# Performance work log

Measured on AMD Instinct MI355X. Metric: run time of the kernel, lower is better.

## Reference

```python
import jax, jax.numpy as jnp
import numpy as np

NP_, NS_ = 100000, 10000      # num pdrugs / seffect nodes
FPD, FSE = 512, 768           # raw feature dims
H = 64                        # hidden_channels
E = 1_600_000                 # message-passing edges
L = 1_000_000                 # labeled edges (pos+neg)


def setup_inputs() -> dict:
    key = jax.random.key(0)
    ks = jax.random.split(key, 40)
    f32 = jnp.float32

    def nrm(k, shape, scale=0.05):
        return jax.random.normal(k, shape, f32) * scale

    inp = {}
    inp['x_pdrugs'] = jax.random.normal(ks[0], (NP_, FPD), f32)
    inp['x_seffect'] = jax.random.normal(ks[1], (NS_, FSE), f32)
    inp['node_id_pd'] = jnp.arange(NP_)
    inp['node_id_se'] = jnp.arange(NS_)
    inp['edge_index'] = jnp.stack([
        jax.random.randint(ks[2], (E,), 0, NP_),
        jax.random.randint(ks[3], (E,), 0, NS_)])
    # positive labeled edges + negative-sampled edges (label 0)
    inp['edge_label_index'] = jnp.stack([
        jax.random.randint(ks[4], (L,), 0, NP_),
        jax.random.randint(ks[5], (L,), 0, NS_)])
    inp['edge_label'] = jnp.concatenate(
        [jnp.ones(L // 2, f32), jnp.zeros(L - L // 2, f32)])

    # input projections + node embeddings
    inp['W_pd'] = nrm(ks[6], (FPD, H)); inp['b_pd'] = jnp.zeros((H,), f32)
    inp['W_se'] = nrm(ks[7], (FSE, H)); inp['b_se'] = jnp.zeros((H,), f32)
    inp['emb_pd'] = nrm(ks[8], (NP_, H), 1.0)
    inp['emb_se'] = nrm(ks[9], (NS_, H), 1.0)

    # hetero SAGEConv params: 2 layers x 2 edge types (p2s, s2p)
    i = 10
    for lyr in (1, 2):
        for et in ('p2s', 's2p'):
            inp[f'c{lyr}_{et}_Wl'] = nrm(ks[i], (H, H)); i += 1
            inp[f'c{lyr}_{et}_bl'] = jnp.zeros((H,), f32)
            inp[f'c{lyr}_{et}_Wr'] = nrm(ks[i], (H, H)); i += 1
    return inp


def _sage(x_src, x_dst, src_idx, dst_idx, n_dst, Wl, bl, Wr):
    # SAGEConv: lin_l(mean_j x_src[j]) + lin_r(x_dst)
    msg = x_src[src_idx]                                   # [E, H] gather
    agg = jax.ops.segment_sum(msg, dst_idx, num_segments=n_dst)
    deg = jax.ops.segment_sum(jnp.ones((src_idx.shape[0],), x_src.dtype),
                              dst_idx, num_segments=n_dst)
    mean = agg / jnp.clip(deg, 1.0)[:, None]
    return mean @ Wl + bl + x_dst @ Wr


def reference(x_pdrugs, x_seffect, edge_label,
              W_pd, b_pd, W_se, b_se, emb_pd, emb_se,
              c1_p2s_Wl, c1_p2s_bl, c1_p2s_Wr,
              c1_s2p_Wl, c1_s2p_bl, c1_s2p_Wr,
              c2_p2s_Wl, c2_p2s_bl, c2_p2s_Wr,
              c2_s2p_Wl, c2_s2p_bl, c2_s2p_Wr,
              node_id_pd, node_id_se, edge_index, edge_label_index):
    src, dst = edge_index[0], edge_index[1]  # pdrugs -> seffect

    # embed + linear fusion
    h_pd = x_pdrugs @ W_pd + b_pd + emb_pd[node_id_pd]
    h_se = x_seffect @ W_se + b_se + emb_se[node_id_se]

    # hetero GNN layer 1 (relu)
    se1 = jax.nn.relu(_sage(h_pd, h_se, src, dst, NS_, c1_p2s_Wl, c1_p2s_bl, c1_p2s_Wr))
    pd1 = jax.nn.relu(_sage(h_se, h_pd, dst, src, NP_, c1_s2p_Wl, c1_s2p_bl, c1_s2p_Wr))

    # hetero GNN layer 2 (no activation)
    se2 = _sage(pd1, se1, src, dst, NS_, c2_p2s_Wl, c2_p2s_bl, c2_p2s_Wr)
    pd2 = _sage(se1, pd1, dst, src, NP_, c2_s2p_Wl, c2_s2p_bl, c2_s2p_Wr)

    # edge-wise gather-dot classifier
    pred = jnp.sum(pd2[edge_label_index[0]] * se2[edge_label_index[1]], axis=-1)
    return (pred, edge_label)
```

## Files before the change

kernel.cpp:

```cpp
#include <hip/hip_runtime.h>

namespace {

constexpr int NP = 100000;
constexpr int NS = 10000;
constexpr int EC = 1600000;
constexpr int LC = 1000000;

constexpr int SH_S = 6;
constexpr int SH_P = 9;
constexpr int NBS = (NS + 63) >> SH_S;
constexpr int NBP = (NP + 511) >> SH_P;
constexpr int CHUNK = 8192;
constexpr int NBLK = (EC + CHUNK - 1) / CHUNK;

typedef short i16x8 __attribute__((ext_vector_type(8)));
typedef float f32x4 __attribute__((ext_vector_type(4)));

__device__ inline ushort f2bf(float f) {
  unsigned u = __float_as_uint(f);
  u += 0x7FFFu + ((u >> 16) & 1u);
  return (ushort)(u >> 16);
}


__global__ void __launch_bounds__(256) k_bcount(const int* __restrict__ src,
                                                const int* __restrict__ dst,
                                                int* __restrict__ bcntS,
                                                int* __restrict__ bcntP, int E) {
  __shared__ int hS[256];
  __shared__ int hP[256];
  const int t = threadIdx.x;
  hS[t] = 0;
  hP[t] = 0;
  __syncthreads();
  const int base = blockIdx.x * CHUNK;
  const int end = min(base + CHUNK, E);
  for (int e = base + t; e < end; e += 256) {
    atomicAdd(&hS[dst[e] >> SH_S], 1);
    atomicAdd(&hP[src[e] >> SH_P], 1);
  }
  __syncthreads();
  if (t < NBS && hS[t]) atomicAdd(&bcntS[t], hS[t]);
  if (t < NBP && hP[t]) atomicAdd(&bcntP[t], hP[t]);
}

__global__ void __launch_bounds__(256) k_bscan(const int* __restrict__ bcntS,
                                               const int* __restrict__ bcntP,
                                               int* __restrict__ gbaseS,
                                               int* __restrict__ gbaseP,
                                               int* __restrict__ gcurS,
                                               int* __restrict__ gcurP) {
  __shared__ int s[256];
  const int t = threadIdx.x;
  int v = (t < NBS) ? bcntS[t] : 0;
  s[t] = v;
  __syncthreads();
  for (int off = 1; off < 256; off <<= 1) {
    int u = (t >= off) ? s[t - off] : 0;
    __syncthreads();
    s[t] += u;
    __syncthreads();
  }
  if (t < NBS) {
    int ex = s[t] - v;
    gbaseS[t] = ex;
    gcurS[t] = ex;
  }
  __syncthreads();
  v = (t < NBP) ? bcntP[t] : 0;
  s[t] = v;
  __syncthreads();
  for (int off = 1; off < 256; off <<= 1) {
    int u = (t >= off) ? s[t - off] : 0;
    __syncthreads();
    s[t] += u;
    __syncthreads();
  }
  if (t < NBP) {
    int ex = s[t] - v;
    gbaseP[t] = ex;
    gcurP[t] = ex;
  }
}

__global__ void __launch_bounds__(256) k_bscatter(const int* __restrict__ src,
                                                  const int* __restrict__ dst,
                                                  int* __restrict__ gcurS,
                                                  int* __restrict__ gcurP,
                                                  int2* __restrict__ tmpS,
                                                  int2* __restrict__ tmpP, int E) {
  __shared__ int hS[256];
  __shared__ int hP[256];
  const int t = threadIdx.x;
  hS[t] = 0;
  hP[t] = 0;
  __syncthreads();
  const int base = blockIdx.x * CHUNK;
  const int end = min(base + CHUNK, E);
  for (int e = base + t; e < end; e += 256) {
    atomicAdd(&hS[dst[e] >> SH_S], 1);
    atomicAdd(&hP[src[e] >> SH_P], 1);
  }
  __syncthreads();
  int myBaseS = 0, myBaseP = 0;
  if (t < NBS) {
    int c = hS[t];
    myBaseS = c ? atomicAdd(&gcurS[t], c) : 0;
  }
  if (t < NBP) {
    int c = hP[t];
    myBaseP = c ? atomicAdd(&gcurP[t], c) : 0;
  }
  __syncthreads();
  if (t < NBS) hS[t] = myBaseS;
  if (t < NBP) hP[t] = myBaseP;
  __syncthreads();
  for (int e = base + t; e < end; e += 256) {
    const int d = dst[e];
    const int s = src[e];
    int p = atomicAdd(&hS[d >> SH_S], 1);
    tmpS[p] = make_int2(d, s);
    int q = atomicAdd(&hP[s >> SH_P], 1);
    tmpP[q] = make_int2(s, d);
  }
}

template <int NN>
__global__ void __launch_bounds__(256) k_bfinal(const int2* __restrict__ tmp,
                                                const int* __restrict__ gbase,
                                                const int* __restrict__ bcnt,
                                                int shift, int Nnodes,
                                                int* __restrict__ rowptr,
                                                int* __restrict__ deg,
                                                int* __restrict__ col) {
  __shared__ int ldeg[NN];
  __shared__ int lscan[512];
  const int b = blockIdx.x;
  const int t = threadIdx.x;
  const int n0 = b << shift;
  const int base = gbase[b];
  const int cnt = bcnt[b];
  for (int i = t; i < NN; i += 256) ldeg[i] = 0;
  __syncthreads();
  for (int j = t; j < cnt; j += 256) atomicAdd(&ldeg[tmp[base + j].x - n0], 1);
  __syncthreads();
  for (int i = t; i < 512; i += 256) lscan[i] = (i < NN) ? ldeg[i] : 0;
  __syncthreads();
  for (int off = 1; off < 512; off <<= 1) {
    const int i0 = t, i1 = t + 256;
    const int v0 = (i0 >= off) ? lscan[i0 - off] : 0;
    const int v1 = (i1 >= off) ? lscan[i1 - off] : 0;
    __syncthreads();
    lscan[i0] += v0;
    lscan[i1] += v1;
    __syncthreads();
  }
  for (int i = t; i < NN; i += 256) {
    const int n = n0 + i;
    if (n < Nnodes) {
      const int dg = ldeg[i];
      rowptr[n] = base + lscan[i] - dg;
      deg[n] = dg;
    }
  }
  __syncthreads();
  for (int i = t; i < NN; i += 256) lscan[i] -= ldeg[i];
  __syncthreads();
  for (int j = t; j < cnt; j += 256) {
    const int2 pr = tmp[base + j];
    const int p = atomicAdd(&lscan[pr.x - n0], 1);
    col[base + p] = pr.y;
  }
}


struct WtJob {
  const float* src;
  ushort* dst;
  int K;
  int stride;
  int off;
};
struct WtJobs {
  WtJob j[10];
};

__global__ void __launch_bounds__(256) k_wt_all(WtJobs jobs) {
  int e = blockIdx.x * 256 + threadIdx.x;
#pragma unroll
  for (int i = 0; i < 10; i++) {
    const int K = jobs.j[i].K;
    const int sz = K * 64;
    if (e < sz) {
      const int n = e / K;
      const int k = e - n * K;
      jobs.j[i].dst[(size_t)n * jobs.j[i].stride + jobs.j[i].off + k] =
          f2bf(jobs.j[i].src[(size_t)k * 64 + n]);
      return;
    }
    e -= sz;
  }
}


template <bool RELU, bool EMB>
__global__ void __launch_bounds__(256) k_mgemm(const float* __restrict__ A0,
                                               const float* __restrict__ A1, int KA0,
                                               int sA0, int sA1, int K,
                                               const ushort* __restrict__ Wt,
                                               const float* __restrict__ bias,
                                               const float* __restrict__ emb,
                                               const int* __restrict__ nid,
                                               float* __restrict__ out, int M) {
  __shared__ ushort Xs[64 * 72];
  __shared__ ushort Ws[64 * 72];
  const int t = threadIdx.x;
  const int row0 = blockIdx.x * 64;
  const int lane = t & 63;
  const int w = t >> 6;
  const int m16 = lane & 15;
  const int q = lane >> 4;

  f32x4 acc[4];
#pragma unroll
  for (int nt = 0; nt < 4; nt++) acc[nt] = {0.f, 0.f, 0.f, 0.f};

  const int ksteps = K >> 6;
  for (int ks = 0; ks < ksteps; ks++) {
    const int k0 = ks << 6;
    float4 xv[4];
#pragma unroll
    for (int i = 0; i < 4; i++) {
      const int u = t + i * 256;
      const int row = u >> 4;
      const int k4 = (u & 15) << 2;
      const int gr = min(row0 + row, M - 1);
      const int kk = k0 + k4;
      const float* sp = (kk < KA0) ? (A0 + (size_t)gr * sA0 + kk)
                                   : (A1 + (size_t)gr * sA1 + (kk - KA0));
      xv[i] = *reinterpret_cast<const float4*>(sp);
    }
    uint4 wv[2];
#pragma unroll
    for (int i = 0; i < 2; i++) {
      const int u = t + i * 256;
      const int n = u >> 3;
      const int kk8 = (u & 7) << 3;
      wv[i] = *reinterpret_cast<const uint4*>(Wt + (size_t)n * K + k0 + kk8);
    }
    __syncthreads();
#pragma unroll
    for (int i = 0; i < 4; i++) {
      const int u = t + i * 256;
      const int row = u >> 4;
      const int k4 = (u & 15) << 2;
      ushort4 o;
      o.x = f2bf(xv[i].x);
      o.y = f2bf(xv[i].y);
      o.z = f2bf(xv[i].z);
      o.w = f2bf(xv[i].w);
      *reinterpret_cast<ushort4*>(&Xs[row * 72 + k4]) = o;
    }
#pragma unroll
    for (int i = 0; i < 2; i++) {
      const int u = t + i * 256;
      const int n = u >> 3;
      const int kk8 = (u & 7) << 3;
      *reinterpret_cast<uint4*>(&Ws[n * 72 + kk8]) = wv[i];
    }
    __syncthreads();

    const ushort* ap = &Xs[(w * 16 + m16) * 72 + q * 8];
    const i16x8 a0 = *reinterpret_cast<const i16x8*>(ap);
    const i16x8 a1 = *reinterpret_cast<const i16x8*>(ap + 32);
#pragma unroll
    for (int nt = 0; nt < 4; nt++) {
      const ushort* bp = &Ws[(nt * 16 + m16) * 72 + q * 8];
      const i16x8 b0 = *reinterpret_cast<const i16x8*>(bp);
      const i16x8 b1 = *reinterpret_cast<const i16x8*>(bp + 32);
      acc[nt] = __builtin_amdgcn_mfma_f32_16x16x32_bf16(a0, b0, acc[nt], 0, 0, 0);
      acc[nt] = __builtin_amdgcn_mfma_f32_16x16x32_bf16(a1, b1, acc[nt], 0, 0, 0);
    }
  }

  int grow[4];
  int nrow[4];
#pragma unroll
  for (int r = 0; r < 4; r++) {
    grow[r] = row0 + w * 16 + q * 4 + r;
    nrow[r] = (EMB && grow[r] < M) ? nid[grow[r]] : 0;
  }
#pragma unroll
  for (int nt = 0; nt < 4; nt++) {
    const int colv = nt * 16 + m16;
    const float bv = bias[colv];
#pragma unroll
    for (int r = 0; r < 4; r++) {
      if (grow[r] < M) {
        float v = acc[nt][r] + bv;
        if (EMB) v += emb[(size_t)nrow[r] * 64 + colv];
        if (RELU) v = fmaxf(v, 0.f);
        out[(size_t)grow[r] * 64 + colv] = v;
      }
    }
  }
}


__global__ void __launch_bounds__(256) k_agg(const float* __restrict__ h,
                                             const int* __restrict__ rowptr,
                                             const int* __restrict__ deg,
                                             const int* __restrict__ col,
                                             float* __restrict__ mean, int n_dst) {
  const int node = blockIdx.x * 4 + (threadIdx.x >> 6);
  const int lane = threadIdx.x & 63;
  if (node >= n_dst) return;
  const int beg = rowptr[node];
  const int cnt = deg[node];
  float acc = 0.f;
  int j = 0;
  for (; j + 8 <= cnt; j += 8) {
    int n0 = col[beg + j + 0], n1 = col[beg + j + 1];
    int n2 = col[beg + j + 2], n3 = col[beg + j + 3];
    int n4 = col[beg + j + 4], n5 = col[beg + j + 5];
    int n6 = col[beg + j + 6], n7 = col[beg + j + 7];
    float a0 = h[(size_t)n0 * 64 + lane];
    float a1 = h[(size_t)n1 * 64 + lane];
    float a2 = h[(size_t)n2 * 64 + lane];
    float a3 = h[(size_t)n3 * 64 + lane];
    float a4 = h[(size_t)n4 * 64 + lane];
    float a5 = h[(size_t)n5 * 64 + lane];
    float a6 = h[(size_t)n6 * 64 + lane];
    float a7 = h[(size_t)n7 * 64 + lane];
    acc += ((a0 + a1) + (a2 + a3)) + ((a4 + a5) + (a6 + a7));
  }
  for (; j < cnt; ++j) acc += h[(size_t)col[beg + j] * 64 + lane];
  const float d = (cnt > 0) ? (float)cnt : 1.f;
  mean[(size_t)node * 64 + lane] = acc / d;
}


__global__ void __launch_bounds__(256) k_classify(const float* __restrict__ pd2,
                                                  const float* __restrict__ se2,
                                                  const int* __restrict__ i0,
                                                  const int* __restrict__ i1,
                                                  float* __restrict__ pred, int L) {
  const int e = blockIdx.x * 16 + (threadIdx.x >> 4);
  if (e >= L) return;
  const int l16 = threadIdx.x & 15;
  const int a = i0[e];
  const int b = i1[e];
  const float4 va = *reinterpret_cast<const float4*>(&pd2[(size_t)a * 64 + l16 * 4]);
  const float4 vb = *reinterpret_cast<const float4*>(&se2[(size_t)b * 64 + l16 * 4]);
  float v = va.x * vb.x + va.y * vb.y + va.z * vb.z + va.w * vb.w;
  v += __shfl_xor(v, 1, 16);
  v += __shfl_xor(v, 2, 16);
  v += __shfl_xor(v, 4, 16);
  v += __shfl_xor(v, 8, 16);
  if (l16 == 0) pred[e] = v;
}

__global__ void k_copy4(const float4* __restrict__ src, float4* __restrict__ dst, int n4) {
  int i = blockIdx.x * blockDim.x + threadIdx.x;
  if (i < n4) dst[i] = src[i];
}

}

extern "C" void kernel_launch(void* const* d_in, const int* in_sizes, int n_in,
                              void* d_out, int out_size, void* d_ws, size_t ws_size,
                              hipStream_t stream) {
  (void)in_sizes; (void)n_in; (void)out_size; (void)ws_size;
  const float* x_pd = (const float*)d_in[0];
  const float* x_se = (const float*)d_in[1];
  const int* nid_pd = (const int*)d_in[2];
  const int* nid_se = (const int*)d_in[3];
  const int* eidx = (const int*)d_in[4];
  const int* elidx = (const int*)d_in[5];
  const float* elabel = (const float*)d_in[6];
  const float* W_pd = (const float*)d_in[7];
  const float* b_pd = (const float*)d_in[8];
  const float* W_se = (const float*)d_in[9];
  const float* b_se = (const float*)d_in[10];
  const float* emb_pd = (const float*)d_in[11];
  const float* emb_se = (const float*)d_in[12];
  const float* c1_p2s_Wl = (const float*)d_in[13];
  const float* c1_p2s_bl = (const float*)d_in[14];
  const float* c1_p2s_Wr = (const float*)d_in[15];
  const float* c1_s2p_Wl = (const float*)d_in[16];
  const float* c1_s2p_bl = (const float*)d_in[17];
  const float* c1_s2p_Wr = (const float*)d_in[18];
  const float* c2_p2s_Wl = (const float*)d_in[19];
  const float* c2_p2s_bl = (const float*)d_in[20];
  const float* c2_p2s_Wr = (const float*)d_in[21];
  const float* c2_s2p_Wl = (const float*)d_in[22];
  const float* c2_s2p_bl = (const float*)d_in[23];
  const float* c2_s2p_Wr = (const float*)d_in[24];

  const int* src = eidx;
  const int* dst = eidx + EC;
  const int* li0 = elidx;
  const int* li1 = elidx + LC;

  char* ws = (char*)d_ws;
  size_t o = 0;
  auto alloc = [&](size_t bytes) -> char* {
    char* p = ws + o;
    o = (o + bytes + 255) & ~(size_t)255;
    return p;
  };
  float* h_pd = (float*)alloc((size_t)NP * 64 * 4);
  float* h_se = (float*)alloc((size_t)NS * 64 * 4);
  float* pd1 = (float*)alloc((size_t)NP * 64 * 4);
  float* se1 = (float*)alloc((size_t)NS * 64 * 4);
  float* agg_pd = (float*)alloc((size_t)NP * 64 * 4);
  float* agg_se = (float*)alloc((size_t)NS * 64 * 4);
  int* col_se = (int*)alloc((size_t)EC * 4);
  int* col_pd = (int*)alloc((size_t)EC * 4);
  int* deg_se = (int*)alloc((size_t)NS * 4);
  int* deg_pd = (int*)alloc((size_t)NP * 4);
  int* rp_se = (int*)alloc((size_t)NS * 4);
  int* rp_pd = (int*)alloc((size_t)NP * 4);
  int* bcntS = (int*)alloc(1024);
  int* bcntP = (int*)alloc(1024);
  int* gbaseS = (int*)alloc(1024);
  int* gbaseP = (int*)alloc(1024);
  int* gcurS = (int*)alloc(1024);
  int* gcurP = (int*)alloc(1024);
  ushort* wt_pd = (ushort*)alloc((size_t)64 * 512 * 2);
  ushort* wt_se = (ushort*)alloc((size_t)64 * 768 * 2);
  ushort* wt_c1p2s = (ushort*)alloc((size_t)64 * 128 * 2);
  ushort* wt_c1s2p = (ushort*)alloc((size_t)64 * 128 * 2);
  ushort* wt_c2p2s = (ushort*)alloc((size_t)64 * 128 * 2);
  ushort* wt_c2s2p = (ushort*)alloc((size_t)64 * 128 * 2);

  int2* tmpS = (int2*)agg_pd;
  int2* tmpP = tmpS + EC;

  hipMemsetAsync(bcntS, 0, 1024, stream);
  hipMemsetAsync(bcntP, 0, 1024, stream);

  k_bcount<<<NBLK, 256, 0, stream>>>(src, dst, bcntS, bcntP, EC);
  k_bscan<<<1, 256, 0, stream>>>(bcntS, bcntP, gbaseS, gbaseP, gcurS, gcurP);
  k_bscatter<<<NBLK, 256, 0, stream>>>(src, dst, gcurS, gcurP, tmpS, tmpP, EC);
  k_bfinal<64><<<NBS, 256, 0, stream>>>(tmpS, gbaseS, bcntS, SH_S, NS, rp_se, deg_se, col_se);
  k_bfinal<512><<<NBP, 256, 0, stream>>>(tmpP, gbaseP, bcntP, SH_P, NP, rp_pd, deg_pd, col_pd);

  {
    WtJobs jobs;
    jobs.j[0] = {W_pd, wt_pd, 512, 512, 0};
    jobs.j[1] = {W_se, wt_se, 768, 768, 0};
    jobs.j[2] = {c1_p2s_Wl, wt_c1p2s, 64, 128, 0};
    jobs.j[3] = {c1_p2s_Wr, wt_c1p2s, 64, 128, 64};
    jobs.j[4] = {c1_s2p_Wl, wt_c1s2p, 64, 128, 0};
    jobs.j[5] = {c1_s2p_Wr, wt_c1s2p, 64, 128, 64};
    jobs.j[6] = {c2_p2s_Wl, wt_c2p2s, 64, 128, 0};
    jobs.j[7] = {c2_p2s_Wr, wt_c2p2s, 64, 128, 64};
    jobs.j[8] = {c2_s2p_Wl, wt_c2s2p, 64, 128, 0};
    jobs.j[9] = {c2_s2p_Wr, wt_c2s2p, 64, 128, 64};
    const int tot = 64 * (512 + 768 + 8 * 64);
    k_wt_all<<<(tot + 255) / 256, 256, 0, stream>>>(jobs);
  }

  const int gP = (NP + 63) / 64;
  const int gS = (NS + 63) / 64;

  k_mgemm<false, true><<<gP, 256, 0, stream>>>(x_pd, nullptr, 512, 512, 0, 512, wt_pd,
                                               b_pd, emb_pd, nid_pd, h_pd, NP);
  k_mgemm<false, true><<<gS, 256, 0, stream>>>(x_se, nullptr, 768, 768, 0, 768, wt_se,
                                               b_se, emb_se, nid_se, h_se, NS);

  k_agg<<<(NS + 3) / 4, 256, 0, stream>>>(h_pd, rp_se, deg_se, col_se, agg_se, NS);
  k_mgemm<true, false><<<gS, 256, 0, stream>>>(agg_se, h_se, 64, 64, 64, 128, wt_c1p2s,
                                               c1_p2s_bl, nullptr, nullptr, se1, NS);
  k_agg<<<(NP + 3) / 4, 256, 0, stream>>>(h_se, rp_pd, deg_pd, col_pd, agg_pd, NP);
  k_mgemm<true, false><<<gP, 256, 0, stream>>>(agg_pd, h_pd, 64, 64, 64, 128, wt_c1s2p,
                                               c1_s2p_bl, nullptr, nullptr, pd1, NP);

  float* se2 = h_se;
  float* pd2 = h_pd;
  k_agg<<<(NS + 3) / 4, 256, 0, stream>>>(pd1, rp_se, deg_se, col_se, agg_se, NS);
  k_mgemm<false, false><<<gS, 256, 0, stream>>>(agg_se, se1, 64, 64, 64, 128, wt_c2p2s,
                                                c2_p2s_bl, nullptr, nullptr, se2, NS);
  k_agg<<<(NP + 3) / 4, 256, 0, stream>>>(se1, rp_pd, deg_pd, col_pd, agg_pd, NP);
  k_mgemm<false, false><<<gP, 256, 0, stream>>>(agg_pd, pd1, 64, 64, 64, 128, wt_c2s2p,
                                                c2_s2p_bl, nullptr, nullptr, pd2, NP);

  float* outF = (float*)d_out;
  k_classify<<<(LC + 15) / 16, 256, 0, stream>>>(pd2, se2, li0, li1, outF, LC);
  k_copy4<<<(LC / 4 + 255) / 256, 256, 0, stream>>>((const float4*)elabel,
                                                    (float4*)(outF + LC), LC / 4);
}
```

Measured before the change: 857.6 us.

## Store intermediates in bf16, pack bucket entries, and batch paired kernels into single launches

Hidden activations (h, layer-1 outputs, aggregated means) are now stored as bf16 instead of fp32. This halves the bytes moved by the neighbor-gather aggregation and the GEMM input reads. Bucket-sort temporaries are packed into one int per edge instead of int2. The paired pd/se GEMMs and aggregations are merged into single launches via job structs, and the label copy is folded into the classifier kernel. This adds bf16 rounding of intermediates, which may affect accuracy, and an extra barrier per k-step in the GEMM loop.

Result: faster. 762.6 us (-11.1%).

```diff
diff --git a/kernel.cpp b/kernel.cpp
--- a/kernel.cpp
+++ b/kernel.cpp
@@ -22,6 +22,8 @@
   u += 0x7FFFu + ((u >> 16) & 1u);
   return (ushort)(u >> 16);
 }
+__device__ inline float bflo(uint v) { return __uint_as_float(v << 16); }
+__device__ inline float bfhi(uint v) { return __uint_as_float(v & 0xffff0000u); }
 
 
 __global__ void __launch_bounds__(256) k_bcount(const int* __restrict__ src,
@@ -88,8 +90,8 @@
                                                   const int* __restrict__ dst,
                                                   int* __restrict__ gcurS,
                                                   int* __restrict__ gcurP,
-                                                  int2* __restrict__ tmpS,
-                                                  int2* __restrict__ tmpP, int E) {
+                                                  int* __restrict__ tmpS,
+                                                  int* __restrict__ tmpP, int E) {
   __shared__ int hS[256];
   __shared__ int hP[256];
   const int t = threadIdx.x;
@@ -120,14 +122,14 @@
     const int d = dst[e];
     const int s = src[e];
     int p = atomicAdd(&hS[d >> SH_S], 1);
-    tmpS[p] = make_int2(d, s);
+    tmpS[p] = ((d & 63) << 17) | s;
     int q = atomicAdd(&hP[s >> SH_P], 1);
-    tmpP[q] = make_int2(s, d);
-  }
-}
-
-template <int NN>
-__global__ void __launch_bounds__(256) k_bfinal(const int2* __restrict__ tmp,
+    tmpP[q] = ((s & 511) << 14) | d;
+  }
+}
+
+template <int NN, int LBITS>
+__global__ void __launch_bounds__(256) k_bfinal(const int* __restrict__ tmp,
                                                 const int* __restrict__ gbase,
                                                 const int* __restrict__ bcnt,
                                                 int shift, int Nnodes,
@@ -143,7 +145,7 @@
   const int cnt = bcnt[b];
   for (int i = t; i < NN; i += 256) ldeg[i] = 0;
   __syncthreads();
-  for (int j = t; j < cnt; j += 256) atomicAdd(&ldeg[tmp[base + j].x - n0], 1);
+  for (int j = t; j < cnt; j += 256) atomicAdd(&ldeg[tmp[base + j] >> LBITS], 1);
   __syncthreads();
   for (int i = t; i < 512; i += 256) lscan[i] = (i < NN) ? ldeg[i] : 0;
   __syncthreads();
@@ -168,9 +170,9 @@
   for (int i = t; i < NN; i += 256) lscan[i] -= ldeg[i];
   __syncthreads();
   for (int j = t; j < cnt; j += 256) {
-    const int2 pr = tmp[base + j];
-    const int p = atomicAdd(&lscan[pr.x - n0], 1);
-    col[base + p] = pr.y;
+    const int v = tmp[base + j];
+    const int p = atomicAdd(&lscan[v >> LBITS], 1);
+    col[base + p] = v & ((1 << LBITS) - 1);
   }
 }
 
@@ -204,23 +206,35 @@
 }
 
 
-template <bool RELU, bool EMB>
-__global__ void __launch_bounds__(256) k_mgemm(const float* __restrict__ A0,
-                                               const float* __restrict__ A1, int KA0,
-                                               int sA0, int sA1, int K,
-                                               const ushort* __restrict__ Wt,
-                                               const float* __restrict__ bias,
-                                               const float* __restrict__ emb,
-                                               const int* __restrict__ nid,
-                                               float* __restrict__ out, int M) {
+struct GJob {
+  const void* A0;
+  const void* A1;
+  int KA0, sA0, sA1, K;
+  const ushort* Wt;
+  const float* bias;
+  const float* emb;
+  const int* nid;
+  void* out;
+  int M;
+  int nblk;
+};
+
+template <bool RELU, bool EMB, bool ABF16, bool OBF16>
+__global__ void __launch_bounds__(256) k_mgemm2(GJob ja, GJob jb) {
   __shared__ ushort Xs[64 * 72];
   __shared__ ushort Ws[64 * 72];
+  const bool sec = (int)blockIdx.x >= ja.nblk;
+  const GJob j = sec ? jb : ja;
+  const int bid = sec ? ((int)blockIdx.x - ja.nblk) : (int)blockIdx.x;
   const int t = threadIdx.x;
-  const int row0 = blockIdx.x * 64;
+  const int row0 = bid * 64;
   const int lane = t & 63;
   const int w = t >> 6;
   const int m16 = lane & 15;
   const int q = lane >> 4;
+  const int M = j.M;
+  const int K = j.K;
+  const int KA0 = j.KA0;
 
   f32x4 acc[4];
 #pragma unroll
@@ -229,38 +243,63 @@
   const int ksteps = K >> 6;
   for (int ks = 0; ks < ksteps; ks++) {
     const int k0 = ks << 6;
-    float4 xv[4];
-#pragma unroll
-    for (int i = 0; i < 4; i++) {
-      const int u = t + i * 256;
-      const int row = u >> 4;
-      const int k4 = (u & 15) << 2;
-      const int gr = min(row0 + row, M - 1);
-      const int kk = k0 + k4;
-      const float* sp = (kk < KA0) ? (A0 + (size_t)gr * sA0 + kk)
-                                   : (A1 + (size_t)gr * sA1 + (kk - KA0));
-      xv[i] = *reinterpret_cast<const float4*>(sp);
-    }
     uint4 wv[2];
 #pragma unroll
     for (int i = 0; i < 2; i++) {
       const int u = t + i * 256;
       const int n = u >> 3;
       const int kk8 = (u & 7) << 3;
-      wv[i] = *reinterpret_cast<const uint4*>(Wt + (size_t)n * K + k0 + kk8);
-    }
-    __syncthreads();
-#pragma unroll
-    for (int i = 0; i < 4; i++) {
-      const int u = t + i * 256;
-      const int row = u >> 4;
-      const int k4 = (u & 15) << 2;
-      ushort4 o;
-      o.x = f2bf(xv[i].x);
-      o.y = f2bf(xv[i].y);
-      o.z = f2bf(xv[i].z);
-      o.w = f2bf(xv[i].w);
-      *reinterpret_cast<ushort4*>(&Xs[row * 72 + k4]) = o;
+      wv[i] = *reinterpret_cast<const uint4*>(j.Wt + (size_t)n * K + k0 + kk8);
+    }
+    if constexpr (ABF16) {
+      uint4 xv[2];
+#pragma unroll
+      for (int i = 0; i < 2; i++) {
+        const int u = t + i * 256;
+        const int row = u >> 3;
+        const int k8 = (u & 7) << 3;
+        const int gr = min(row0 + row, M - 1);
+        const int kk = k0 + k8;
+        const ushort* sp = (kk < KA0)
+                               ? ((const ushort*)j.A0 + (size_t)gr * j.sA0 + kk)
+                               : ((const ushort*)j.A1 + (size_t)gr * j.sA1 + (kk - KA0));
+        xv[i] = *reinterpret_cast<const uint4*>(sp);
+      }
+      __syncthreads();
+#pragma unroll
+      for (int i = 0; i < 2; i++) {
+        const int u = t + i * 256;
+        const int row = u >> 3;
+        const int k8 = (u & 7) << 3;
+        *reinterpret_cast<uint4*>(&Xs[row * 72 + k8]) = xv[i];
+      }
+    } else {
+      float4 xv[4];
+#pragma unroll
+      for (int i = 0; i < 4; i++) {
+        const int u = t + i * 256;
+        const int row = u >> 4;
+        const int k4 = (u & 15) << 2;
+        const int gr = min(row0 + row, M - 1);
+        const int kk = k0 + k4;
+        const float* sp = (kk < KA0)
+                              ? ((const float*)j.A0 + (size_t)gr * j.sA0 + kk)
+                              : ((const float*)j.A1 + (size_t)gr * j.sA1 + (kk - KA0));
+        xv[i] = *reinterpret_cast<const float4*>(sp);
+      }
+      __syncthreads();
+#pragma unroll
+      for (int i = 0; i < 4; i++) {
+        const int u = t + i * 256;
+        const int row = u >> 4;
+        const int k4 = (u & 15) << 2;
+        ushort4 o;
+        o.x = f2bf(xv[i].x);
+        o.y = f2bf(xv[i].y);
+        o.z = f2bf(xv[i].z);
+        o.w = f2bf(xv[i].w);
+        *reinterpret_cast<ushort4*>(&Xs[row * 72 + k4]) = o;
+      }
     }
 #pragma unroll
     for (int i = 0; i < 2; i++) {
@@ -282,6 +321,7 @@
       acc[nt] = __builtin_amdgcn_mfma_f32_16x16x32_bf16(a0, b0, acc[nt], 0, 0, 0);
       acc[nt] = __builtin_amdgcn_mfma_f32_16x16x32_bf16(a1, b1, acc[nt], 0, 0, 0);
     }
+    __syncthreads();
   }
 
   int grow[4];
@@ -289,55 +329,86 @@
 #pragma unroll
   for (int r = 0; r < 4; r++) {
     grow[r] = row0 + w * 16 + q * 4 + r;
-    nrow[r] = (EMB && grow[r] < M) ? nid[grow[r]] : 0;
+    nrow[r] = (EMB && grow[r] < M) ? j.nid[grow[r]] : 0;
   }
 #pragma unroll
   for (int nt = 0; nt < 4; nt++) {
     const int colv = nt * 16 + m16;
-    const float bv = bias[colv];
+    const float bv = j.bias[colv];
 #pragma unroll
     for (int r = 0; r < 4; r++) {
       if (grow[r] < M) {
         float v = acc[nt][r] + bv;
-        if (EMB) v += emb[(size_t)nrow[r] * 64 + colv];
+        if (EMB) v += j.emb[(size_t)nrow[r] * 64 + colv];
         if (RELU) v = fmaxf(v, 0.f);
-        out[(size_t)grow[r] * 64 + colv] = v;
+        if (OBF16)
+          ((ushort*)j.out)[(size_t)grow[r] * 64 + colv] = f2bf(v);
+        else
+          ((float*)j.out)[(size_t)grow[r] * 64 + colv] = v;
       }
     }
   }
 }
 
 
-__global__ void __launch_bounds__(256) k_agg(const float* __restrict__ h,
-                                             const int* __restrict__ rowptr,
-                                             const int* __restrict__ deg,
-                                             const int* __restrict__ col,
-                                             float* __restrict__ mean, int n_dst) {
-  const int node = blockIdx.x * 4 + (threadIdx.x >> 6);
+__global__ void __launch_bounds__(256) k_agg2(
+    const ushort* __restrict__ hS,
+    const ushort* __restrict__ hP,
+    const int* __restrict__ rpS, const int* __restrict__ degS, const int* __restrict__ colS,
+    const int* __restrict__ rpP, const int* __restrict__ degP, const int* __restrict__ colP,
+    ushort* __restrict__ outS,
+    ushort* __restrict__ outP
+) {
+  int g = blockIdx.x * 4 + (threadIdx.x >> 6);
+  const uint* hu;
+  const int* rp;
+  const int* deg;
+  const int* col;
+  uint* out;
+  int node;
+  if (g < NS) {
+    hu = (const uint*)hS; rp = rpS; deg = degS; col = colS; out = (uint*)outS;
+    node = g;
+  } else {
+    node = g - NS;
+    if (node >= NP) return;
+    hu = (const uint*)hP; rp = rpP; deg = degP; col = colP; out = (uint*)outP;
+  }
   const int lane = threadIdx.x & 63;
-  if (node >= n_dst) return;
-  const int beg = rowptr[node];
+  const int c = lane & 31;
+  const int half = lane >> 5;
+  const int beg = rp[node];
   const int cnt = deg[node];
-  float acc = 0.f;
-  int j = 0;
-  for (; j + 8 <= cnt; j += 8) {
-    int n0 = col[beg + j + 0], n1 = col[beg + j + 1];
-    int n2 = col[beg + j + 2], n3 = col[beg + j + 3];
-    int n4 = col[beg + j + 4], n5 = col[beg + j + 5];
-    int n6 = col[beg + j + 6], n7 = col[beg + j + 7];
-    float a0 = h[(size_t)n0 * 64 + lane];
-    float a1 = h[(size_t)n1 * 64 + lane];
-    float a2 = h[(size_t)n2 * 64 + lane];
-    float a3 = h[(size_t)n3 * 64 + lane];
-    float a4 = h[(size_t)n4 * 64 + lane];
-    float a5 = h[(size_t)n5 * 64 + lane];
-    float a6 = h[(size_t)n6 * 64 + lane];
-    float a7 = h[(size_t)n7 * 64 + lane];
-    acc += ((a0 + a1) + (a2 + a3)) + ((a4 + a5) + (a6 + a7));
-  }
-  for (; j < cnt; ++j) acc += h[(size_t)col[beg + j] * 64 + lane];
-  const float d = (cnt > 0) ? (float)cnt : 1.f;
-  mean[(size_t)node * 64 + lane] = acc / d;
+  float a0 = 0.f, a1 = 0.f;
+  int jj = 0;
+  for (; jj + 16 <= cnt; jj += 16) {
+    int n[8];
+#pragma unroll
+    for (int u = 0; u < 8; u++) n[u] = col[beg + jj + 2 * u + half];
+#pragma unroll
+    for (int u = 0; u < 8; u++) {
+      const uint v = hu[(size_t)n[u] * 32 + c];
+      a0 += bflo(v);
+      a1 += bfhi(v);
+    }
+  }
+  for (; jj + 2 <= cnt; jj += 2) {
+    const uint v = hu[(size_t)col[beg + jj + half] * 32 + c];
+    a0 += bflo(v);
+    a1 += bfhi(v);
+  }
+  if (jj < cnt && half == 0) {
+    const uint v = hu[(size_t)col[beg + jj] * 32 + c];
+    a0 += bflo(v);
+    a1 += bfhi(v);
+  }
+  a0 += __shfl_xor(a0, 32);
+  a1 += __shfl_xor(a1, 32);
+  if (half == 0) {
+    const float d = (cnt > 0) ? (float)cnt : 1.f;
+    const uint o = (uint)f2bf(a0 / d) | ((uint)f2bf(a1 / d) << 16);
+    out[(size_t)node * 32 + c] = o;
+  }
 }
 
 
@@ -345,7 +416,16 @@
                                                   const float* __restrict__ se2,
                                                   const int* __restrict__ i0,
                                                   const int* __restrict__ i1,
-                                                  float* __restrict__ pred, int L) {
+                                                  const float* __restrict__ elabel,
+                                                  float* __restrict__ outF, int L,
+                                                  int nClsBlk) {
+  if ((int)blockIdx.x >= nClsBlk) {
+    const int i = ((int)blockIdx.x - nClsBlk) * 256 + threadIdx.x;
+    if (i < L / 4)
+      reinterpret_cast<float4*>(outF + L)[i] =
+          reinterpret_cast<const float4*>(elabel)[i];
+    return;
+  }
   const int e = blockIdx.x * 16 + (threadIdx.x >> 4);
   if (e >= L) return;
   const int l16 = threadIdx.x & 15;
@@ -358,12 +438,7 @@
   v += __shfl_xor(v, 2, 16);
   v += __shfl_xor(v, 4, 16);
   v += __shfl_xor(v, 8, 16);
-  if (l16 == 0) pred[e] = v;
-}
-
-__global__ void k_copy4(const float4* __restrict__ src, float4* __restrict__ dst, int n4) {
-  int i = blockIdx.x * blockDim.x + threadIdx.x;
-  if (i < n4) dst[i] = src[i];
+  if (l16 == 0) outF[e] = v;
 }
 
 }
@@ -410,12 +485,14 @@
     o = (o + bytes + 255) & ~(size_t)255;
     return p;
   };
-  float* h_pd = (float*)alloc((size_t)NP * 64 * 4);
-  float* h_se = (float*)alloc((size_t)NS * 64 * 4);
-  float* pd1 = (float*)alloc((size_t)NP * 64 * 4);
-  float* se1 = (float*)alloc((size_t)NS * 64 * 4);
-  float* agg_pd = (float*)alloc((size_t)NP * 64 * 4);
-  float* agg_se = (float*)alloc((size_t)NS * 64 * 4);
+  ushort* h_pd = (ushort*)alloc((size_t)NP * 64 * 2);
+  ushort* h_se = (ushort*)alloc((size_t)NS * 64 * 2);
+  ushort* pd1 = (ushort*)alloc((size_t)NP * 64 * 2);
+  ushort* se1 = (ushort*)alloc((size_t)NS * 64 * 2);
+  ushort* agg_pd = (ushort*)alloc((size_t)NP * 64 * 2);
+  ushort* agg_se = (ushort*)alloc((size_t)NS * 64 * 2);
+  float* pd2 = (float*)alloc((size_t)NP * 64 * 4);
+  float* se2 = (float*)alloc((size_t)NS * 64 * 4);
   int* col_se = (int*)alloc((size_t)EC * 4);
   int* col_pd = (int*)alloc((size_t)EC * 4);
   int* deg_se = (int*)alloc((size_t)NS * 4);
@@ -435,8 +512,8 @@
   ushort* wt_c2p2s = (ushort*)alloc((size_t)64 * 128 * 2);
   ushort* wt_c2s2p = (ushort*)alloc((size_t)64 * 128 * 2);
 
-  int2* tmpS = (int2*)agg_pd;
-  int2* tmpP = tmpS + EC;
+  int* tmpS = (int*)pd2;
+  int* tmpP = tmpS + EC;
 
   hipMemsetAsync(bcntS, 0, 1024, stream);
   hipMemsetAsync(bcntP, 0, 1024, stream);
@@ -444,8 +521,10 @@
   k_bcount<<<NBLK, 256, 0, stream>>>(src, dst, bcntS, bcntP, EC);
   k_bscan<<<1, 256, 0, stream>>>(bcntS, bcntP, gbaseS, gbaseP, gcurS, gcurP);
   k_bscatter<<<NBLK, 256, 0, stream>>>(src, dst, gcurS, gcurP, tmpS, tmpP, EC);
-  k_bfinal<64><<<NBS, 256, 0, stream>>>(tmpS, gbaseS, bcntS, SH_S, NS, rp_se, deg_se, col_se);
-  k_bfinal<512><<<NBP, 256, 0, stream>>>(tmpP, gbaseP, bcntP, SH_P, NP, rp_pd, deg_pd, col_pd);
+  k_bfinal<64, 17><<<NBS, 256, 0, stream>>>(tmpS, gbaseS, bcntS, SH_S, NS, rp_se,
+                                            deg_se, col_se);
+  k_bfinal<512, 14><<<NBP, 256, 0, stream>>>(tmpP, gbaseP, bcntP, SH_P, NP, rp_pd,
+                                             deg_pd, col_pd);
 
   {
     WtJobs jobs;
@@ -465,30 +544,33 @@
 
   const int gP = (NP + 63) / 64;
   const int gS = (NS + 63) / 64;
-
-  k_mgemm<false, true><<<gP, 256, 0, stream>>>(x_pd, nullptr, 512, 512, 0, 512, wt_pd,
-                                               b_pd, emb_pd, nid_pd, h_pd, NP);
-  k_mgemm<false, true><<<gS, 256, 0, stream>>>(x_se, nullptr, 768, 768, 0, 768, wt_se,
-                                               b_se, emb_se, nid_se, h_se, NS);
-
-  k_agg<<<(NS + 3) / 4, 256, 0, stream>>>(h_pd, rp_se, deg_se, col_se, agg_se, NS);
-  k_mgemm<true, false><<<gS, 256, 0, stream>>>(agg_se, h_se, 64, 64, 64, 128, wt_c1p2s,
-                                               c1_p2s_bl, nullptr, nullptr, se1, NS);
-  k_agg<<<(NP + 3) / 4, 256, 0, stream>>>(h_se, rp_pd, deg_pd, col_pd, agg_pd, NP);
-  k_mgemm<true, false><<<gP, 256, 0, stream>>>(agg_pd, h_pd, 64, 64, 64, 128, wt_c1s2p,
-                                               c1_s2p_bl, nullptr, nullptr, pd1, NP);
-
-  float* se2 = h_se;
-  float* pd2 = h_pd;
-  k_agg<<<(NS + 3) / 4, 256, 0, stream>>>(pd1, rp_se, deg_se, col_se, agg_se, NS);
-  k_mgemm<false, false><<<gS, 256, 0, stream>>>(agg_se, se1, 64, 64, 64, 128, wt_c2p2s,
-                                                c2_p2s_bl, nullptr, nullptr, se2, NS);
-  k_agg<<<(NP + 3) / 4, 256, 0, stream>>>(se1, rp_pd, deg_pd, col_pd, agg_pd, NP);
-  k_mgemm<false, false><<<gP, 256, 0, stream>>>(agg_pd, pd1, 64, 64, 64, 128, wt_c2s2p,
-                                                c2_s2p_bl, nullptr, nullptr, pd2, NP);
+  const int gAgg = (NS + NP) / 4;
+
+  {
+    GJob jp = {x_pd, nullptr, 512, 512, 0, 512, wt_pd, b_pd, emb_pd, nid_pd, h_pd, NP, gP};
+    GJob js = {x_se, nullptr, 768, 768, 0, 768, wt_se, b_se, emb_se, nid_se, h_se, NS, gS};
+    k_mgemm2<false, true, false, true><<<gP + gS, 256, 0, stream>>>(jp, js);
+  }
+
+  k_agg2<<<gAgg, 256, 0, stream>>>(h_pd, h_se, rp_se, deg_se, col_se, rp_pd, deg_pd,
+                                   col_pd, agg_se, agg_pd);
+  {
+    GJob jp = {agg_pd, h_pd, 64, 64, 64, 128, wt_c1s2p, c1_s2p_bl, nullptr, nullptr, pd1, NP, gP};
+    GJob js = {agg_se, h_se, 64, 64, 64, 128, wt_c1p2s, c1_p2s_bl, nullptr, nullptr, se1, NS, gS};
+    k_mgemm2<true, false, true, true><<<gP + gS, 256, 0, stream>>>(jp, js);
+  }
+
+  k_agg2<<<gAgg, 256, 0, stream>>>(pd1, se1, rp_se, deg_se, col_se, rp_pd, deg_pd,
+                                   col_pd, agg_se, agg_pd);
+  {
+    GJob jp = {agg_pd, pd1, 64, 64, 64, 128, wt_c2s2p, c2_s2p_bl, nullptr, nullptr, pd2, NP, gP};
+    GJob js = {agg_se, se1, 64, 64, 64, 128, wt_c2p2s, c2_p2s_bl, nullptr, nullptr, se2, NS, gS};
+    k_mgemm2<false, false, true, false><<<gP + gS, 256, 0, stream>>>(jp, js);
+  }
 
   float* outF = (float*)d_out;
-  k_classify<<<(LC + 15) / 16, 256, 0, stream>>>(pd2, se2, li0, li1, outF, LC);
-  k_copy4<<<(LC / 4 + 255) / 256, 256, 0, stream>>>((const float4*)elabel,
-                                                    (float4*)(outF + LC), LC / 4);
-}
+  const int nClsBlk = (LC + 15) / 16;
+  const int nCpyBlk = (LC / 4 + 255) / 256;
+  k_classify<<<nClsBlk + nCpyBlk, 256, 0, stream>>>(pd2, se2, li0, li1, elabel, outF,
+                                                    LC, nClsBlk);
+}
```
